# Optimization experiments

Measured on AMD Instinct MI355X. Metric: run time of the kernel, lower is better.

## Reference

```python
import jax, jax.numpy as jnp
import numpy as np
import math

HEADS = 4
DK = 64            # dim // heads
TEMP = 1.0
LMAX = 2048        # max segment length (for padded ragged attention)


def setup_inputs() -> dict:
    key = jax.random.key(0)
    ks = jax.random.split(key, 6)
    T, H, B = 1024, 256, 16
    # ragged lengths alternating 2048/1024 -> N = 24576
    lengths = np.tile(np.array([2048, 1024], dtype=np.int64), B // 2)
    N = int(lengths.sum())
    s = 1.0 / math.sqrt(H)
    return {
        "go_mat": jax.random.normal(ks[0], (T, H), jnp.float32),
        "node_h": jax.random.normal(ks[1], (N, H), jnp.float32),
        "Wq": jax.random.normal(ks[2], (H, H), jnp.float32) * s,
        "Wk": jax.random.normal(ks[3], (H, H), jnp.float32) * s,
        "Wv": jax.random.normal(ks[4], (H, H), jnp.float32) * s,
        "Wproj": jax.random.normal(ks[5], (H, H), jnp.float32) * s,
        "num_nodes_per_graph": jnp.asarray(lengths),
    }


def reference(go_mat, node_h, Wq, Wk, Wv, Wproj, num_nodes_per_graph):
    lengths = num_nodes_per_graph
    B = lengths.shape[0]
    N, H = node_h.shape
    T = go_mat.shape[0]

    # segment bookkeeping: graph id and within-graph offset for each node
    cum = jnp.cumsum(lengths)                       # [B]
    starts = cum - lengths                          # [B]
    g = jnp.searchsorted(cum, jnp.arange(N), side="right")  # [N] graph id
    off = jnp.arange(N) - starts[g]                 # [N] position within graph

    # projections (torch Linear: x @ W.T)
    Q = (go_mat @ Wq.T).reshape(T, HEADS, DK).transpose(1, 0, 2)   # [h,T,dk]
    K = node_h @ Wk.T                                              # [N,H]
    V = node_h @ Wv.T

    # scatter packed nodes into padded [B, Lmax, H]
    Kp = jnp.zeros((B, LMAX, H), K.dtype).at[g, off].set(K)
    Vp = jnp.zeros((B, LMAX, H), V.dtype).at[g, off].set(V)
    Kp = Kp.reshape(B, LMAX, HEADS, DK).transpose(0, 2, 1, 3)      # [B,h,L,dk]
    Vp = Vp.reshape(B, LMAX, HEADS, DK).transpose(0, 2, 1, 3)

    scores = jnp.einsum("htd,bhld->bhtl", Q, Kp) / (math.sqrt(DK) * TEMP)
    valid = jnp.arange(LMAX)[None, :] < lengths[:, None]           # [B,L]
    scores = jnp.where(valid[:, None, None, :], scores, jnp.float32(-1e30))
    attn = jax.nn.softmax(scores, axis=-1)                         # [B,h,T,L]

    ctx = jnp.einsum("bhtl,bhld->bhtd", attn, Vp)                  # [B,h,T,dk]
    ctx = ctx.transpose(0, 2, 1, 3).reshape(B, T, H)               # [B,T,H]
    return ctx @ Wproj.T
```

## Files before the change

kernel.cpp:

```cpp
#include <hip/hip_runtime.h>
#include <math.h>

#define HEADS 4
#define DK 64
#define HD 256

typedef __attribute__((ext_vector_type(8))) __bf16 bf16x8;
typedef __attribute__((ext_vector_type(4))) float floatx4;

__device__ __forceinline__ ushort f2bf(float f) {
  union { float f; unsigned u; } x; x.f = f;
  return (ushort)((x.u + 0x7FFF + ((x.u >> 16) & 1)) >> 16);
}

#if __has_builtin(__builtin_amdgcn_exp2f)
#define EXP2(x) __builtin_amdgcn_exp2f(x)
#else
#define EXP2(x) exp2f(x)
#endif

__device__ __forceinline__ unsigned cvtpk_bf16(float lo, float hi) {
  unsigned r;
  asm("v_cvt_pk_bf16_f32 %0, %1, %2" : "=v"(r) : "v"(lo), "v"(hi));
  return r;
}

#define GLDS(g, l) __builtin_amdgcn_global_load_lds(                      \
    (const __attribute__((address_space(1))) unsigned*)(g),               \
    (__attribute__((address_space(3))) unsigned*)(l), 16, 0, 0)

__global__ __launch_bounds__(256) void cvt_fused(
    const float* __restrict__ go, const float* __restrict__ nh,
    const float* __restrict__ w0, const float* __restrict__ w1,
    const float* __restrict__ w2, const float* __restrict__ w3,
    ushort* __restrict__ gobf, ushort* __restrict__ nodebf,
    ushort* __restrict__ wbf, int T, int N) {
  const int idx = blockIdx.x * 256 + threadIdx.x;
  const int row = idx >> 5, gr = idx & 31;
  if (row >= T + N + 4 * 256) return;
  const float* x; ushort* y; int r = row;
  if (row < T) { x = go; y = gobf; }
  else if (row < T + N) { x = nh; y = nodebf; r = row - T; }
  else {
    const int wr = row - T - N, wi = wr >> 8;
    r = wr & 255;
    x = (wi == 0) ? w0 : (wi == 1) ? w1 : (wi == 2) ? w2 : w3;
    y = wbf + (size_t)wi * HD * HD;
  }
  const int chunk = gr >> 3, g = gr & 7;
  const float* src = x + (size_t)r * 256 + gr * 8;
  float4 a = *(const float4*)src;
  float4 bq = *(const float4*)(src + 4);
  ushort* dst = y + (size_t)r * 256 + chunk * 64 + (g ^ (r & 7)) * 8;
  union { ushort4 h[2]; uint4 q; } pk;
  pk.h[0] = (ushort4){f2bf(a.x), f2bf(a.y), f2bf(a.z), f2bf(a.w)};
  pk.h[1] = (ushort4){f2bf(bq.x), f2bf(bq.y), f2bf(bq.z), f2bf(bq.w)};
  *(uint4*)dst = pk.q;
}

template <int NW>
__device__ __forceinline__ void gemm_tile(const ushort* __restrict__ A,
                                          const ushort* __restrict__ W,
                                          ushort* __restrict__ C, int m0,
                                          int n0, int mode, int ldc,
                                          ushort* As, ushort* Ws, int lane,
                                          int w, int quad, int l15) {
  const int wm = w & 1, wn = w >> 1;
  floatx4 acc[4][NW];
#pragma unroll
  for (int mt = 0; mt < 4; ++mt)
#pragma unroll
    for (int nt = 0; nt < NW; ++nt) acc[mt][nt] = (floatx4){0.f, 0.f, 0.f, 0.f};

  for (int k0 = 0; k0 < 256; k0 += 64) {
    __syncthreads();
#pragma unroll
    for (int t = 0; t < 4; ++t)
      GLDS(A + (size_t)(m0 + w * 32 + t * 8 + (lane >> 3)) * 256 + k0 + (lane & 7) * 8,
           &As[(w * 32 + t * 8) * 64]);
#pragma unroll
    for (int t = 0; t < NW; ++t)
      GLDS(W + (size_t)(n0 + w * (8 * NW) + t * 8 + (lane >> 3)) * 256 + k0 + (lane & 7) * 8,
           &Ws[(w * (8 * NW) + t * 8) * 64]);
    __syncthreads();

#pragma unroll
    for (int kk = 0; kk < 2; ++kk) {
      const int pg = ((kk * 4 + quad) ^ (l15 & 7)) * 8;
      bf16x8 af[4], bfr[NW];
#pragma unroll
      for (int mt = 0; mt < 4; ++mt)
        af[mt] = *(const bf16x8*)&As[(wm * 64 + mt * 16 + l15) * 64 + pg];
#pragma unroll
      for (int nt = 0; nt < NW; ++nt)
        bfr[nt] = *(const bf16x8*)&Ws[(wn * (16 * NW) + nt * 16 + l15) * 64 + pg];
#pragma unroll
      for (int mt = 0; mt < 4; ++mt)
#pragma unroll
        for (int nt = 0; nt < NW; ++nt)
          acc[mt][nt] = __builtin_amdgcn_mfma_f32_16x16x32_bf16(
              af[mt], bfr[nt], acc[mt][nt], 0, 0, 0);
    }
  }

#pragma unroll
  for (int mt = 0; mt < 4; ++mt)
#pragma unroll
    for (int nt = 0; nt < NW; ++nt) {
      const int col = n0 + wn * (16 * NW) + nt * 16 + l15;
      if (mode == 2) {
        const int d = col & 63;
        const int g = mt * 2 + (quad >> 1);
        const int node = m0 + wm * 64 + (g ^ (d & 7)) * 8 + (quad & 1) * 4;
        ushort4 o = {f2bf(acc[mt][nt][0]), f2bf(acc[mt][nt][1]),
                     f2bf(acc[mt][nt][2]), f2bf(acc[mt][nt][3])};
        *(ushort4*)&C[(size_t)col * ldc + node] = o;
      } else {
#pragma unroll
        for (int r = 0; r < 4; ++r) {
          const int row = m0 + wm * 64 + mt * 16 + quad * 4 + r;
          if (mode == 3) {
            ((float*)C)[(size_t)row * 256 + col] = acc[mt][nt][r];
          } else {
            int cc = col;
            if (mode == 1)
              cc = (col & ~63) | (((((col >> 3) & 7) ^ (row & 7))) << 3) | (col & 7);
            C[(size_t)row * 256 + cc] = f2bf(acc[mt][nt][r]);
          }
        }
      }
    }
}

__global__ __launch_bounds__(256) void qkv_gemm(const ushort* __restrict__ gobf,
                                                const ushort* __restrict__ nodebf,
                                                const ushort* __restrict__ wbf,
                                                ushort* __restrict__ Qbf,
                                                ushort* __restrict__ Kgb,
                                                ushort* __restrict__ Vtb,
                                                int T, int N) {
  __shared__ __align__(16) ushort As[128 * 64];
  __shared__ __align__(16) ushort Ws[128 * 64];
  const int tid = threadIdx.x, lane = tid & 63, w = tid >> 6;
  const int quad = lane >> 4, l15 = lane & 15;
  const int QX = T >> 7, KB = N >> 7;
  const int NT = QX + 2 * KB;
  const int jx = blockIdx.x % NT;
  const int n0 = (blockIdx.x / NT) * 128;
  if (jx < QX)
    gemm_tile<4>(gobf, wbf, Qbf, jx * 128, n0, 0, 0, As, Ws, lane, w, quad, l15);
  else if (jx < QX + KB)
    gemm_tile<4>(nodebf, wbf + (size_t)HD * HD, Kgb, (jx - QX) * 128, n0, 1, 0,
                 As, Ws, lane, w, quad, l15);
  else
    gemm_tile<4>(nodebf, wbf + (size_t)2 * HD * HD, Vtb, (jx - QX - KB) * 128,
                 n0, 2, N, As, Ws, lane, w, quad, l15);
}

__global__ __launch_bounds__(256, 3) void attn_split(
    const ushort* __restrict__ Qb, const ushort* __restrict__ Kg,
    const ushort* __restrict__ Vt, const int* __restrict__ lens,
    float* __restrict__ Opart, float* __restrict__ Lpart,
    int T, int N, int B) {
  __shared__ __align__(16) ushort Ks[2][64 * 64];
  __shared__ __align__(16) ushort Vs[2][64 * 64];

  const int tid = threadIdx.x, lane = tid & 63, wave = tid >> 6;
  const int quad = lane >> 4, l15 = lane & 15;
  const int QX = T >> 7;
  const int nspl = N >> 10;
  const int grpc = HEADS * nspl;
  const int qx = blockIdx.x / grpc;
  const int rem = blockIdx.x - qx * grpc;
  const int h = rem / nspl;
  const int zid = rem - h * nspl;

  int z = zid, b, start = 0, len = 0, off = -1;
  for (b = 0; b < B; ++b) {
    len = lens[b];
    const int s = (len + 1023) >> 10;
    if (z < s) { off = z << 10; break; }
    z -= s; start += len;
  }
  if (off < 0) return;
  const int kcnt = min(1024, len - off);
  const int kbeg = start + off;

  for (int i = (int)(blockIdx.x >> 8); i > 0; --i)
    __builtin_amdgcn_s_sleep(35);

  const int q0 = qx * 128 + wave * 32;
  bf16x8 qb[2][2];
#pragma unroll
  for (int qt = 0; qt < 2; ++qt)
#pragma unroll
    for (int kk = 0; kk < 2; ++kk)
      qb[qt][kk] = *(const bf16x8*)(Qb + (size_t)(q0 + qt * 16 + l15) * 256 +
                                    h * 64 + kk * 32 + quad * 8);

  floatx4 o[2][4];
#pragma unroll
  for (int qt = 0; qt < 2; ++qt)
#pragma unroll
    for (int nt = 0; nt < 4; ++nt) o[qt][nt] = (floatx4){0.f, 0.f, 0.f, 0.f};
  float lsum[2] = {0.f, 0.f};

  const float sc = 0.18033688011112042f;
  const int srow = lane >> 3;
  const int scol = (lane & 7) * 8;

  GLDS(Kg + (size_t)(kbeg + wave * 8 + srow) * 256 + h * 64 + scol,
       &Ks[0][(wave * 8) * 64]);
  GLDS(Kg + (size_t)(kbeg + wave * 8 + 32 + srow) * 256 + h * 64 + scol,
       &Ks[0][(wave * 8 + 32) * 64]);
  GLDS(Vt + (size_t)(h * 64 + wave * 8 + srow) * (size_t)N + kbeg + scol,
       &Vs[0][(wave * 8) * 64]);
  GLDS(Vt + (size_t)(h * 64 + wave * 8 + 32 + srow) * (size_t)N + kbeg + scol,
       &Vs[0][(wave * 8 + 32) * 64]);

  int buf = 0;
  for (int j0 = 0; j0 < kcnt; j0 += 64, buf ^= 1) {
    __syncthreads();
    const int jn = j0 + 64;
    if (jn < kcnt) {
      GLDS(Kg + (size_t)(kbeg + jn + wave * 8 + srow) * 256 + h * 64 + scol,
           &Ks[buf ^ 1][(wave * 8) * 64]);
      GLDS(Kg + (size_t)(kbeg + jn + wave * 8 + 32 + srow) * 256 + h * 64 + scol,
           &Ks[buf ^ 1][(wave * 8 + 32) * 64]);
      GLDS(Vt + (size_t)(h * 64 + wave * 8 + srow) * (size_t)N + kbeg + jn + scol,
           &Vs[buf ^ 1][(wave * 8) * 64]);
      GLDS(Vt + (size_t)(h * 64 + wave * 8 + 32 + srow) * (size_t)N + kbeg + jn + scol,
           &Vs[buf ^ 1][(wave * 8 + 32) * 64]);
    }

    floatx4 st[4][2];
#pragma unroll
    for (int t = 0; t < 4; ++t)
#pragma unroll
      for (int qt = 0; qt < 2; ++qt) st[t][qt] = (floatx4){0.f, 0.f, 0.f, 0.f};
    __builtin_amdgcn_s_setprio(1);
#pragma unroll
    for (int kk = 0; kk < 2; ++kk) {
#pragma unroll
      for (int t = 0; t < 4; ++t) {
        bf16x8 kf = *(const bf16x8*)&Ks[buf][(t * 16 + l15) * 64 +
                                            ((kk * 4 + quad) ^ (l15 & 7)) * 8];
        st[t][0] = __builtin_amdgcn_mfma_f32_16x16x32_bf16(kf, qb[0][kk], st[t][0], 0, 0, 0);
        st[t][1] = __builtin_amdgcn_mfma_f32_16x16x32_bf16(kf, qb[1][kk], st[t][1], 0, 0, 0);
      }
    }
    __builtin_amdgcn_s_setprio(0);

    unsigned W[4][2][2];
    if (jn <= kcnt) {
#pragma unroll
      for (int t = 0; t < 4; ++t)
#pragma unroll
        for (int qt = 0; qt < 2; ++qt) {
          float p[4];
#pragma unroll
          for (int r = 0; r < 4; ++r) p[r] = EXP2(fmaf(st[t][qt][r], sc, -32.0f));
          lsum[qt] += (p[0] + p[1]) + (p[2] + p[3]);
          W[t][qt][0] = cvtpk_bf16(p[0], p[1]);
          W[t][qt][1] = cvtpk_bf16(p[2], p[3]);
        }
    } else {
#pragma unroll
      for (int t = 0; t < 4; ++t)
#pragma unroll
        for (int qt = 0; qt < 2; ++qt) {
          float p[4];
#pragma unroll
          for (int r = 0; r < 4; ++r) {
            const bool v = (j0 + t * 16 + quad * 4 + r) < kcnt;
            p[r] = v ? EXP2(fmaf(st[t][qt][r], sc, -32.0f)) : 0.0f;
          }
          lsum[qt] += (p[0] + p[1]) + (p[2] + p[3]);
          W[t][qt][0] = cvtpk_bf16(p[0], p[1]);
          W[t][qt][1] = cvtpk_bf16(p[2], p[3]);
        }
    }

#pragma unroll
    for (int ks = 0; ks < 2; ++ks) {
      bf16x8 pa[2];
#pragma unroll
      for (int qt = 0; qt < 2; ++qt) {
        unsigned a0 = W[2 * ks][qt][0], a1 = W[2 * ks][qt][1];
        unsigned b0 = W[2 * ks + 1][qt][0], b1 = W[2 * ks + 1][qt][1];
        asm("v_permlane32_swap_b32 %0, %1" : "+v"(a0), "+v"(b0));
        asm("v_permlane32_swap_b32 %0, %1" : "+v"(a1), "+v"(b1));
        asm("v_permlane16_swap_b32 %0, %1" : "+v"(a0), "+v"(b0));
        asm("v_permlane16_swap_b32 %0, %1" : "+v"(a1), "+v"(b1));
        union { uint4 u; bf16x8 v; } c;
        c.u = make_uint4(a0, a1, b0, b1);
        pa[qt] = c.v;
      }
      __builtin_amdgcn_s_setprio(1);
#pragma unroll
      for (int nt = 0; nt < 4; ++nt) {
        bf16x8 vf = *(const bf16x8*)&Vs[buf][(nt * 16 + l15) * 64 +
                                            ((ks * 4 + quad) ^ (l15 & 7)) * 8];
        o[0][nt] = __builtin_amdgcn_mfma_f32_16x16x32_bf16(pa[0], vf, o[0][nt], 0, 0, 0);
        o[1][nt] = __builtin_amdgcn_mfma_f32_16x16x32_bf16(pa[1], vf, o[1][nt], 0, 0, 0);
      }
      __builtin_amdgcn_s_setprio(0);
    }
  }

  const int part = (zid * HEADS + h) * QX + qx;
  float* op = Opart + (size_t)part * 8192;
#pragma unroll
  for (int qt = 0; qt < 2; ++qt) {
#pragma unroll
    for (int nt = 0; nt < 4; ++nt)
#pragma unroll
      for (int r = 0; r < 4; ++r)
        op[(wave * 32 + qt * 16 + quad * 4 + r) * 64 + nt * 16 + l15] = o[qt][nt][r];
    float lt = lsum[qt];
    lt += __shfl_xor(lt, 16);
    lt += __shfl_xor(lt, 32);
    if (lane < 16)
      Lpart[(size_t)part * 128 + wave * 32 + qt * 16 + lane] = lt;
  }
}

__global__ __launch_bounds__(256) void combine(const float* __restrict__ Opart,
                                               const float* __restrict__ Lpart,
                                               const int* __restrict__ lens,
                                               ushort* __restrict__ ctxb, int T) {
  const int t = threadIdx.x;
  const int row = blockIdx.x * 64 + (t >> 2);
  const int h = t & 3;
  const int b = row / T;
  const int tq = row - b * T;
  const int qx = tq >> 7, qr = tq & 127;
  const int QX = T >> 7;
  int z0 = 0;
  for (int i = 0; i < b; ++i) z0 += (lens[i] + 1023) >> 10;
  const int ns = (lens[b] + 1023) >> 10;

  float l = 0.f;
  float4 acc[16];
#pragma unroll
  for (int g = 0; g < 16; ++g) acc[g] = make_float4(0.f, 0.f, 0.f, 0.f);
  for (int s = 0; s < ns; ++s) {
    const size_t part = (size_t)((z0 + s) * HEADS + h) * QX + qx;
    l += Lpart[part * 128 + qr];
    const float4* src = (const float4*)(Opart + part * 8192 + (size_t)qr * 64);
#pragma unroll
    for (int g = 0; g < 16; ++g) {
      float4 v = src[g];
      acc[g].x += v.x; acc[g].y += v.y; acc[g].z += v.z; acc[g].w += v.w;
    }
  }
  const float inv = 1.0f / l;
  ushort* dst = ctxb + (size_t)row * 256 + h * 64;
#pragma unroll
  for (int gg = 0; gg < 8; ++gg) {
    const float4 a = acc[gg * 2], c = acc[gg * 2 + 1];
    const int phys = gg ^ (row & 7);
    ushort4 o0 = {f2bf(a.x * inv), f2bf(a.y * inv), f2bf(a.z * inv), f2bf(a.w * inv)};
    ushort4 o1 = {f2bf(c.x * inv), f2bf(c.y * inv), f2bf(c.z * inv), f2bf(c.w * inv)};
    *(ushort4*)&dst[phys * 8] = o0;
    *(ushort4*)&dst[phys * 8 + 4] = o1;
  }
}

__global__ __launch_bounds__(256) void proj_gemm(const ushort* __restrict__ ctxb,
                                                 const ushort* __restrict__ wbf,
                                                 float* __restrict__ outp) {
  __shared__ __align__(16) ushort As[128 * 64];
  __shared__ __align__(16) ushort Ws[64 * 64];
  const int tid = threadIdx.x, lane = tid & 63, w = tid >> 6;
  const int quad = lane >> 4, l15 = lane & 15;
  gemm_tile<2>(ctxb, wbf + (size_t)3 * HD * HD, (ushort*)outp, blockIdx.x * 128,
               blockIdx.y * 64, 3, 0, As, Ws, lane, w, quad, l15);
}

extern "C" void kernel_launch(void* const* d_in, const int* in_sizes, int n_in,
                              void* d_out, int out_size, void* d_ws, size_t ws_size,
                              hipStream_t stream) {
  const float* go     = (const float*)d_in[0];
  const float* node_h = (const float*)d_in[1];
  const float* Wq     = (const float*)d_in[2];
  const float* Wk     = (const float*)d_in[3];
  const float* Wv     = (const float*)d_in[4];
  const float* Wproj  = (const float*)d_in[5];
  const int*   lens   = (const int*)d_in[6];

  const int T = in_sizes[0] / HD;
  const int N = in_sizes[1] / HD;
  const int B = in_sizes[6];
  const int NSPL = N >> 10;
  const int QX = T >> 7;
  const int KB = N >> 7;

  char* p = (char*)d_ws;
  ushort* Kgb  = (ushort*)p;  p += (size_t)N * HD * 2;
  ushort* Vtb  = (ushort*)p;  p += (size_t)N * HD * 2;
  ushort* Qbf  = (ushort*)p;  p += (size_t)T * HD * 2;
  ushort* gobf = (ushort*)p;  p += (size_t)T * HD * 2;
  ushort* ctxb = (ushort*)p;  p += (size_t)B * T * HD * 2;
  ushort* wbf  = (ushort*)p;  p += (size_t)4 * HD * HD * 2;
  ushort* nodebf = (ushort*)p;
  float* Opart = (float*)p;   p += (size_t)NSPL * HEADS * QX * 8192 * 4;
  float* Lpart = (float*)p;   p += (size_t)NSPL * HEADS * QX * 128 * 4;

  cvt_fused<<<((T + N + 1024) * 32 + 255) / 256, 256, 0, stream>>>(
      go, node_h, Wq, Wk, Wv, Wproj, gobf, nodebf, wbf, T, N);

  qkv_gemm<<<(QX + 2 * KB) * 2, 256, 0, stream>>>(gobf, nodebf, wbf, Qbf, Kgb,
                                                  Vtb, T, N);

  attn_split<<<QX * HEADS * NSPL, 256, 0, stream>>>(Qbf, Kgb, Vtb, lens,
                                                    Opart, Lpart, T, N, B);

  combine<<<(B * T) / 64, 256, 0, stream>>>(Opart, Lpart, lens, ctxb, T);

  proj_gemm<<<dim3((B * T) / 128, 4), 256, 0, stream>>>(ctxb, wbf, (float*)d_out);
}
```

Baseline: 155.7 us.

## Fuse split-combine with output projection GEMM in one kernel

Merges the combine kernel and the projection GEMM so each block reduces the attention partials for 64 rows into a bf16 context tile in LDS. It then multiplies that tile by Wproj, loaded in 64-column chunks, and writes fp32 output directly. This removes the global ctx round-trip and one kernel launch. In exchange it uses 64KB of LDS per block, which may limit occupancy, and Wproj is reloaded by every block.

```diff
diff --git a/kernel.cpp b/kernel.cpp
--- a/kernel.cpp
+++ b/kernel.cpp
@@ -119,14 +119,10 @@
 #pragma unroll
         for (int r = 0; r < 4; ++r) {
           const int row = m0 + wm * 64 + mt * 16 + quad * 4 + r;
-          if (mode == 3) {
-            ((float*)C)[(size_t)row * 256 + col] = acc[mt][nt][r];
-          } else {
-            int cc = col;
-            if (mode == 1)
-              cc = (col & ~63) | (((((col >> 3) & 7) ^ (row & 7))) << 3) | (col & 7);
-            C[(size_t)row * 256 + cc] = f2bf(acc[mt][nt][r]);
-          }
+          int cc = col;
+          if (mode == 1)
+            cc = (col & ~63) | (((((col >> 3) & 7) ^ (row & 7))) << 3) | (col & 7);
+          C[(size_t)row * 256 + cc] = f2bf(acc[mt][nt][r]);
         }
       }
     }
@@ -325,57 +321,86 @@
   }
 }
 
-__global__ __launch_bounds__(256) void combine(const float* __restrict__ Opart,
-                                               const float* __restrict__ Lpart,
-                                               const int* __restrict__ lens,
-                                               ushort* __restrict__ ctxb, int T) {
+__global__ __launch_bounds__(256) void combine_proj(
+    const float* __restrict__ Opart, const float* __restrict__ Lpart,
+    const int* __restrict__ lens, const ushort* __restrict__ wproj,
+    float* __restrict__ outp, int T) {
+  __shared__ __align__(16) ushort Cs[64 * 256];
+  __shared__ __align__(16) ushort Ws[64 * 256];
+
   const int t = threadIdx.x;
-  const int row = blockIdx.x * 64 + (t >> 2);
-  const int h = t & 3;
-  const int b = row / T;
-  const int tq = row - b * T;
-  const int qx = tq >> 7, qr = tq & 127;
-  const int QX = T >> 7;
-  int z0 = 0;
-  for (int i = 0; i < b; ++i) z0 += (lens[i] + 1023) >> 10;
-  const int ns = (lens[b] + 1023) >> 10;
-
-  float l = 0.f;
-  float4 acc[16];
-#pragma unroll
-  for (int g = 0; g < 16; ++g) acc[g] = make_float4(0.f, 0.f, 0.f, 0.f);
-  for (int s = 0; s < ns; ++s) {
-    const size_t part = (size_t)((z0 + s) * HEADS + h) * QX + qx;
-    l += Lpart[part * 128 + qr];
-    const float4* src = (const float4*)(Opart + part * 8192 + (size_t)qr * 64);
-#pragma unroll
-    for (int g = 0; g < 16; ++g) {
-      float4 v = src[g];
-      acc[g].x += v.x; acc[g].y += v.y; acc[g].z += v.z; acc[g].w += v.w;
-    }
-  }
-  const float inv = 1.0f / l;
-  ushort* dst = ctxb + (size_t)row * 256 + h * 64;
-#pragma unroll
-  for (int gg = 0; gg < 8; ++gg) {
-    const float4 a = acc[gg * 2], c = acc[gg * 2 + 1];
-    const int phys = gg ^ (row & 7);
-    ushort4 o0 = {f2bf(a.x * inv), f2bf(a.y * inv), f2bf(a.z * inv), f2bf(a.w * inv)};
-    ushort4 o1 = {f2bf(c.x * inv), f2bf(c.y * inv), f2bf(c.z * inv), f2bf(c.w * inv)};
-    *(ushort4*)&dst[phys * 8] = o0;
-    *(ushort4*)&dst[phys * 8 + 4] = o1;
-  }
-}
-
-__global__ __launch_bounds__(256) void proj_gemm(const ushort* __restrict__ ctxb,
-                                                 const ushort* __restrict__ wbf,
-                                                 float* __restrict__ outp) {
-  __shared__ __align__(16) ushort As[128 * 64];
-  __shared__ __align__(16) ushort Ws[64 * 64];
-  const int tid = threadIdx.x, lane = tid & 63, w = tid >> 6;
+  {
+    const int lrow = t >> 2;
+    const int h = t & 3;
+    const int row = blockIdx.x * 64 + lrow;
+    const int b = row / T;
+    const int tq = row - b * T;
+    const int qx = tq >> 7, qr = tq & 127;
+    const int QX = T >> 7;
+    int z0 = 0;
+    for (int i = 0; i < b; ++i) z0 += (lens[i] + 1023) >> 10;
+    const int ns = (lens[b] + 1023) >> 10;
+
+    float l = 0.f;
+    float4 acc[16];
+#pragma unroll
+    for (int g = 0; g < 16; ++g) acc[g] = make_float4(0.f, 0.f, 0.f, 0.f);
+    for (int s = 0; s < ns; ++s) {
+      const size_t part = (size_t)((z0 + s) * HEADS + h) * QX + qx;
+      l += Lpart[part * 128 + qr];
+      const float4* src = (const float4*)(Opart + part * 8192 + (size_t)qr * 64);
+#pragma unroll
+      for (int g = 0; g < 16; ++g) {
+        float4 v = src[g];
+        acc[g].x += v.x; acc[g].y += v.y; acc[g].z += v.z; acc[g].w += v.w;
+      }
+    }
+    const float inv = 1.0f / l;
+    ushort* dst = &Cs[lrow * 256 + h * 64];
+#pragma unroll
+    for (int gg = 0; gg < 8; ++gg) {
+      const float4 a = acc[gg * 2], c = acc[gg * 2 + 1];
+      const int phys = gg ^ (lrow & 7);
+      ushort4 o0 = {f2bf(a.x * inv), f2bf(a.y * inv), f2bf(a.z * inv), f2bf(a.w * inv)};
+      ushort4 o1 = {f2bf(c.x * inv), f2bf(c.y * inv), f2bf(c.z * inv), f2bf(c.w * inv)};
+      *(ushort4*)&dst[phys * 8] = o0;
+      *(ushort4*)&dst[phys * 8 + 4] = o1;
+    }
+  }
+
+  const int lane = t & 63, w = t >> 6;
   const int quad = lane >> 4, l15 = lane & 15;
-  gemm_tile<2>(ctxb, wbf + (size_t)3 * HD * HD, (ushort*)outp, blockIdx.x * 128,
-               blockIdx.y * 64, 3, 0, As, Ws, lane, w, quad, l15);
+  const size_t row0 = (size_t)blockIdx.x * 64;
+
+  for (int n0c = 0; n0c < 256; n0c += 64) {
+    __syncthreads();
+#pragma unroll
+    for (int tt = 0; tt < 8; ++tt)
+      GLDS(wproj + (size_t)(n0c + w * 16 + tt * 2 + (lane >> 5)) * 256 + (lane & 31) * 8,
+           &Ws[(w * 16 + tt * 2) * 256]);
+    __syncthreads();
+
+    floatx4 oacc[4];
+#pragma unroll
+    for (int nt = 0; nt < 4; ++nt) oacc[nt] = (floatx4){0.f, 0.f, 0.f, 0.f};
+#pragma unroll
+    for (int c = 0; c < 4; ++c)
+#pragma unroll
+      for (int kk = 0; kk < 2; ++kk) {
+        const int pg = ((kk * 4 + quad) ^ (l15 & 7)) * 8;
+        bf16x8 af = *(const bf16x8*)&Cs[(w * 16 + l15) * 256 + c * 64 + pg];
+#pragma unroll
+        for (int nt = 0; nt < 4; ++nt) {
+          bf16x8 bfr = *(const bf16x8*)&Ws[(nt * 16 + l15) * 256 + c * 64 + pg];
+          oacc[nt] = __builtin_amdgcn_mfma_f32_16x16x32_bf16(af, bfr, oacc[nt], 0, 0, 0);
+        }
+      }
+#pragma unroll
+    for (int nt = 0; nt < 4; ++nt)
+#pragma unroll
+      for (int r = 0; r < 4; ++r)
+        outp[(row0 + w * 16 + quad * 4 + r) * 256 + n0c + nt * 16 + l15] = oacc[nt][r];
+  }
 }
 
 extern "C" void kernel_launch(void* const* d_in, const int* in_sizes, int n_in,
@@ -406,6 +431,7 @@
   ushort* nodebf = (ushort*)p;
   float* Opart = (float*)p;   p += (size_t)NSPL * HEADS * QX * 8192 * 4;
   float* Lpart = (float*)p;   p += (size_t)NSPL * HEADS * QX * 128 * 4;
+  (void)ctxb;
 
   cvt_fused<<<((T + N + 1024) * 32 + 255) / 256, 256, 0, stream>>>(
       go, node_h, Wq, Wk, Wv, Wproj, gobf, nodebf, wbf, T, N);
@@ -416,7 +442,7 @@
   attn_split<<<QX * HEADS * NSPL, 256, 0, stream>>>(Qbf, Kgb, Vtb, lens,
                                                     Opart, Lpart, T, N, B);
 
-  combine<<<(B * T) / 64, 256, 0, stream>>>(Opart, Lpart, lens, ctxb, T);
-
-  proj_gemm<<<dim3((B * T) / 128, 4), 256, 0, stream>>>(ctxb, wbf, (float*)d_out);
-}
+  combine_proj<<<(B * T) / 64, 256, 0, stream>>>(Opart, Lpart, lens,
+                                                 wbf + (size_t)3 * HD * HD,
+                                                 (float*)d_out, T);
+}
```

Result: faster. 152.5 us (-2.0%).
